# Performance work log

Measured on AMD Instinct MI355X. Metric: run time of the kernel, lower is better.

The kernel has to match this reference:

```python
import jax, jax.numpy as jnp
import numpy as np

D_MODEL = 1024
NHEAD = 16
D_HEAD = D_MODEL // NHEAD


def setup_inputs() -> dict:
    key = jax.random.key(0)
    ks = jax.random.split(key, 9)
    B, S = 2, 2048
    scale = 1.0 / np.sqrt(D_MODEL)
    x = jax.random.normal(ks[0], (B, S, D_MODEL), dtype=jnp.float32)
    Wq = jax.random.normal(ks[1], (D_MODEL, D_MODEL), dtype=jnp.float32) * scale
    Wk = jax.random.normal(ks[2], (D_MODEL, D_MODEL), dtype=jnp.float32) * scale
    Wv = jax.random.normal(ks[3], (D_MODEL, D_MODEL), dtype=jnp.float32) * scale
    Wo = jax.random.normal(ks[4], (D_MODEL, D_MODEL), dtype=jnp.float32) * scale
    bq = jax.random.normal(ks[5], (D_MODEL,), dtype=jnp.float32) * 0.01
    bk = jax.random.normal(ks[6], (D_MODEL,), dtype=jnp.float32) * 0.01
    bv = jax.random.normal(ks[7], (D_MODEL,), dtype=jnp.float32) * 0.01
    bo = jax.random.normal(ks[8], (D_MODEL,), dtype=jnp.float32) * 0.01
    return {"x": x, "Wq": Wq, "bq": bq, "Wk": Wk, "bk": bk,
            "Wv": Wv, "bv": bv, "Wo": Wo, "bo": bo}


def reference(x, Wq, bq, Wk, bk, Wv, bv, Wo, bo):
    B, S, D = x.shape
    H, Dh = NHEAD, D_HEAD
    # projections; weights stored as (in, out) so y = x @ W + b
    def split_heads(t):  # [B,S,D] -> [B,H,S,Dh]
        return t.reshape(B, S, H, Dh).transpose(0, 2, 1, 3)
    q = split_heads(x @ Wq + bq)
    k = split_heads(x @ Wk + bk)
    v = split_heads(x @ Wv + bv)
    scale = 1.0 / jnp.sqrt(jnp.asarray(Dh, dtype=x.dtype))
    attn = jnp.einsum("bhqd,bhkd->bhqk", q, k) * scale  # [B,H,S,S]
    attn = jax.nn.softmax(attn, axis=-1)
    out = jnp.einsum("bhqk,bhkd->bhqd", attn, v)  # [B,H,S,Dh]
    out = out.transpose(0, 2, 1, 3).reshape(B, S, D)
    return out @ Wo + bo
```

## Files before the change

kernel.cpp:

```cpp
#include <hip/hip_runtime.h>
#include <hip/hip_bf16.h>
#include <stdint.h>
#include <stddef.h>

typedef __bf16 b16;
typedef __bf16 b16x4 __attribute__((ext_vector_type(4)));
typedef __bf16 b16x8 __attribute__((ext_vector_type(8)));
typedef float  f32x4 __attribute__((ext_vector_type(4)));

#define LOG2E 1.4426950408889634f
#define QSCALE (0.125f * LOG2E)

#if __has_builtin(__builtin_amdgcn_exp2f)
#define EXP2F(x) __builtin_amdgcn_exp2f(x)
#else
#define EXP2F(x) exp2f(x)
#endif

typedef __attribute__((address_space(1))) void gvoid;
typedef __attribute__((address_space(3))) void svoid;

__device__ __forceinline__ void async_cp16(void* lds, const void* g) {
    __builtin_amdgcn_global_load_lds((gvoid*)(void*)g, (svoid*)lds, 16, 0, 0);
}

__global__ __launch_bounds__(256) void k_cvt_x(const float* __restrict__ x,
                                               b16* __restrict__ xb) {
    int i = (blockIdx.x * 256 + threadIdx.x) * 4;
    float4 v = *(const float4*)(x + i);
    b16x4 o = { (b16)v.x, (b16)v.y, (b16)v.z, (b16)v.w };
    *(b16x4*)(xb + i) = o;
}

__global__ __launch_bounds__(256) void k_transpose(const float* __restrict__ Wq,
                                                   const float* __restrict__ Wk,
                                                   const float* __restrict__ Wv,
                                                   const float* __restrict__ Wo,
                                                   b16* __restrict__ WtQKV,
                                                   b16* __restrict__ Wot) {
    __shared__ float t[32][33];
    const int z = blockIdx.z;
    const float* W = (z == 0) ? Wq : (z == 1) ? Wk : (z == 2) ? Wv : Wo;
    const int k0 = blockIdx.x * 32, n0 = blockIdx.y * 32;
    const int tr = threadIdx.x >> 3, tc4 = (threadIdx.x & 7) * 4;
    float4 v = *(const float4*)(W + (size_t)(k0 + tr) * 1024 + n0 + tc4);
    t[tr][tc4 + 0] = v.x; t[tr][tc4 + 1] = v.y;
    t[tr][tc4 + 2] = v.z; t[tr][tc4 + 3] = v.w;
    __syncthreads();
    b16* dst = (z < 3) ? (WtQKV + ((size_t)z << 20)) : Wot;
    b16x4 o = { (b16)t[tc4 + 0][tr], (b16)t[tc4 + 1][tr],
                (b16)t[tc4 + 2][tr], (b16)t[tc4 + 3][tr] };
    *(b16x4*)(dst + (size_t)(n0 + tr) * 1024 + k0 + tc4) = o;
}

__device__ __forceinline__ void gemm128_core(const b16* __restrict__ Ab,
                                             const b16* __restrict__ Bb,
                                             b16* As, b16* Bs, int tid,
                                             f32x4 acc[4][4]) {
    const int lane = tid & 63, wave = tid >> 6;
    const int wm = wave & 1, wn = wave >> 1;
    const int quad = lane >> 4, lc = lane & 15;
    const int ci0 = tid, ci1 = tid + 256;
    for (int k0 = 0; k0 < 1024; k0 += 32) {
        __syncthreads();
        async_cp16(As + ci0 * 8, Ab + (ci0 >> 2) * 1024 + k0 + (ci0 & 3) * 8);
        async_cp16(As + ci1 * 8, Ab + (ci1 >> 2) * 1024 + k0 + (ci1 & 3) * 8);
        async_cp16(Bs + ci0 * 8, Bb + (ci0 >> 2) * 1024 + k0 + (ci0 & 3) * 8);
        async_cp16(Bs + ci1 * 8, Bb + (ci1 >> 2) * 1024 + k0 + (ci1 & 3) * 8);
        __syncthreads();
        b16x8 af[4], bfr[4];
#pragma unroll
        for (int mt = 0; mt < 4; ++mt)
            af[mt] = *(const b16x8*)(As + (wm * 64 + mt * 16 + lc) * 32 + quad * 8);
#pragma unroll
        for (int nt = 0; nt < 4; ++nt)
            bfr[nt] = *(const b16x8*)(Bs + (wn * 64 + nt * 16 + lc) * 32 + quad * 8);
#pragma unroll
        for (int mt = 0; mt < 4; ++mt)
#pragma unroll
            for (int nt = 0; nt < 4; ++nt)
                acc[mt][nt] = __builtin_amdgcn_mfma_f32_16x16x32_bf16(
                    af[mt], bfr[nt], acc[mt][nt], 0, 0, 0);
    }
}

__global__ __launch_bounds__(256, 2) void k_gemm_qkv(
    const b16* __restrict__ A, const b16* __restrict__ Bt,
    const float* __restrict__ bq, const float* __restrict__ bk,
    const float* __restrict__ bv,
    b16* __restrict__ Qg, b16* __restrict__ Kg, b16* __restrict__ Vtg) {
    __shared__ __align__(16) b16 As[128 * 32];
    __shared__ __align__(16) b16 Bs[128 * 32];
    const int bm = blockIdx.x, bn = blockIdx.y;
    const int tid = threadIdx.x;
    const int lane = tid & 63, wave = tid >> 6;
    const int wm = wave & 1, wn = wave >> 1;
    const int quad = lane >> 4, lc = lane & 15;

    f32x4 acc[4][4] = {};
    gemm128_core(A + (size_t)(bm * 128) * 1024, Bt + (size_t)(bn * 128) * 1024,
                 As, Bs, tid, acc);

    const int mat = bn >> 3;
    const float* bp = (mat == 0) ? bq : (mat == 1) ? bk : bv;
#pragma unroll
    for (int nt = 0; nt < 4; ++nt) {
        const int n = bn * 128 + wn * 64 + nt * 16 + lc;
        const int cm = n & 1023;
        const int h = cm >> 6, dh = cm & 63;
        const float bval = bp[cm];
#pragma unroll
        for (int mt = 0; mt < 4; ++mt) {
            const int m0 = bm * 128 + wm * 64 + mt * 16 + quad * 4;
            const int b = m0 >> 11;
            const int bh = b * 16 + h;
            const int s0 = m0 & 2047;
            if (mat == 2) {
                b16x4 o;
#pragma unroll
                for (int r = 0; r < 4; ++r) o[r] = (b16)(acc[mt][nt][r] + bval);
                *(b16x4*)(Vtg + (size_t)(bh * 64 + dh) * 2048 + s0) = o;
            } else if (mat == 0) {
#pragma unroll
                for (int r = 0; r < 4; ++r)
                    Qg[(size_t)(bh * 2048 + s0 + r) * 64 + dh] =
                        (b16)((acc[mt][nt][r] + bval) * QSCALE);
            } else {
#pragma unroll
                for (int r = 0; r < 4; ++r)
                    Kg[(size_t)(bh * 2048 + s0 + r) * 64 + dh] =
                        (b16)(acc[mt][nt][r] + bval);
            }
        }
    }
}

__global__ __launch_bounds__(256, 2) void k_flash(
    const b16* __restrict__ Qg, const b16* __restrict__ Kg,
    const b16* __restrict__ Vtg,
    float* __restrict__ Opart, float* __restrict__ lpart,
    b16* __restrict__ AO, int ktiles, int direct) {
    __shared__ __align__(16) b16 Ks[64 * 64];
    __shared__ __align__(16) b16 Vs[64 * 64];
    __shared__ __align__(16) b16 Ps[256 * 72];
    const int qb = blockIdx.x;
    const int bh = blockIdx.y;
    const int part = blockIdx.z;
    const int tid = threadIdx.x, lane = tid & 63, wave = tid >> 6;
    const int quad = lane >> 4, lc = lane & 15;

    const b16* Qbase = Qg + ((size_t)bh * 2048 + qb * 256 + wave * 64) * 64;
    b16x8 qf[4][2];
#pragma unroll
    for (int qt = 0; qt < 4; ++qt)
#pragma unroll
        for (int ch = 0; ch < 2; ++ch)
            qf[qt][ch] = *(const b16x8*)(Qbase + (qt * 16 + lc) * 64 + ch * 32 + quad * 8);

    f32x4 oacc[4][4] = {};
    float lsum[4] = {0.f, 0.f, 0.f, 0.f};

    const b16* Kbh = Kg + (size_t)bh * 2048 * 64;
    const b16* Vbh = Vtg + (size_t)bh * 64 * 2048;
    b16* Pw = Ps + wave * (64 * 72);
    const int kt0 = part * ktiles;

    for (int kt = kt0; kt < kt0 + ktiles; ++kt) {
        __syncthreads();
#pragma unroll
        for (int i = 0; i < 2; ++i) {
            const int ci = tid + i * 256;
            const int r = ci >> 3, cs = ci & 7;
            const int gc = cs ^ (r & 7);
            async_cp16(Ks + ci * 8, Kbh + (size_t)(kt * 64 + r) * 64 + gc * 8);
            async_cp16(Vs + ci * 8, Vbh + (size_t)r * 2048 + kt * 64 + gc * 8);
        }
        __syncthreads();

#pragma unroll
        for (int m = 0; m < 4; ++m) {
            b16x8 kf[2];
#pragma unroll
            for (int ch = 0; ch < 2; ++ch) {
                const int row = m * 16 + lc;
                const int chunk = (ch * 4 + quad) ^ (row & 7);
                kf[ch] = *(const b16x8*)(Ks + row * 64 + chunk * 8);
            }
#pragma unroll
            for (int qt = 0; qt < 4; ++qt) {
                f32x4 s = {};
                s = __builtin_amdgcn_mfma_f32_16x16x32_bf16(kf[0], qf[qt][0], s, 0, 0, 0);
                s = __builtin_amdgcn_mfma_f32_16x16x32_bf16(kf[1], qf[qt][1], s, 0, 0, 0);
                float e0 = EXP2F(s[0]), e1 = EXP2F(s[1]);
                float e2 = EXP2F(s[2]), e3 = EXP2F(s[3]);
                lsum[qt] += (e0 + e1) + (e2 + e3);
                b16x4 p = { (b16)e0, (b16)e1, (b16)e2, (b16)e3 };
                *(b16x4*)(Pw + (qt * 16 + lc) * 72 + m * 16 + quad * 4) = p;
            }
        }

#pragma unroll
        for (int ks = 0; ks < 2; ++ks) {
            b16x8 vf[4], pf[4];
#pragma unroll
            for (int dt = 0; dt < 4; ++dt) {
                const int row = dt * 16 + lc;
                const int chunk = (ks * 4 + quad) ^ (row & 7);
                vf[dt] = *(const b16x8*)(Vs + row * 64 + chunk * 8);
            }
#pragma unroll
            for (int mt = 0; mt < 4; ++mt)
                pf[mt] = *(const b16x8*)(Pw + (mt * 16 + lc) * 72 + ks * 32 + quad * 8);
#pragma unroll
            for (int mt = 0; mt < 4; ++mt)
#pragma unroll
                for (int dt = 0; dt < 4; ++dt)
                    oacc[mt][dt] = __builtin_amdgcn_mfma_f32_16x16x32_bf16(
                        pf[mt], vf[dt], oacc[mt][dt], 0, 0, 0);
        }
    }

#pragma unroll
    for (int qt = 0; qt < 4; ++qt) {
        lsum[qt] += __shfl_xor(lsum[qt], 16, 64);
        lsum[qt] += __shfl_xor(lsum[qt], 32, 64);
    }

    if (!direct) {
        float* Op = Opart + ((size_t)(part * 32 + bh) * 2048 + qb * 256 + wave * 64) * 64;
#pragma unroll
        for (int mt = 0; mt < 4; ++mt)
#pragma unroll
            for (int dt = 0; dt < 4; ++dt)
#pragma unroll
                for (int r = 0; r < 4; ++r)
                    Op[(mt * 16 + quad * 4 + r) * 64 + dt * 16 + lc] = oacc[mt][dt][r];
        if (quad == 0) {
            float* lp = lpart + (size_t)(part * 32 + bh) * 2048 + qb * 256 + wave * 64;
#pragma unroll
            for (int qt = 0; qt < 4; ++qt) lp[qt * 16 + lc] = lsum[qt];
        }
    } else {
        float* Ls = (float*)(void*)Pw;
        if (quad == 0) {
#pragma unroll
            for (int qt = 0; qt < 4; ++qt) Ls[qt * 16 + lc] = lsum[qt];
        }
        const int b = bh >> 4, h = bh & 15;
#pragma unroll
        for (int mt = 0; mt < 4; ++mt)
#pragma unroll
            for (int r = 0; r < 4; ++r) {
                const float inv = 1.0f / Ls[mt * 16 + quad * 4 + r];
                const int s = qb * 256 + wave * 64 + mt * 16 + quad * 4 + r;
#pragma unroll
                for (int dt = 0; dt < 4; ++dt)
                    AO[(size_t)(b * 2048 + s) * 1024 + h * 64 + dt * 16 + lc] =
                        (b16)(oacc[mt][dt][r] * inv);
            }
    }
}

__global__ __launch_bounds__(256) void k_merge(const float* __restrict__ Opart,
                                               const float* __restrict__ lpart,
                                               b16* __restrict__ AO, int np) {
    const int bh = blockIdx.y;
    const int q = blockIdx.x * 16 + (threadIdx.x >> 4);
    const int d4 = (threadIdx.x & 15) * 4;
    const size_t qi = (size_t)bh * 2048 + q;
    f32x4 o = *(const f32x4*)(Opart + qi * 64 + d4);
    float l = lpart[qi];
    if (np == 2) {
        o += *(const f32x4*)(Opart + (qi + (size_t)32 * 2048) * 64 + d4);
        l += lpart[qi + (size_t)32 * 2048];
    }
    const float inv = 1.0f / l;
    const int b = bh >> 4, h = bh & 15;
    b16x4 ob = { (b16)(o[0] * inv), (b16)(o[1] * inv),
                 (b16)(o[2] * inv), (b16)(o[3] * inv) };
    *(b16x4*)(AO + (size_t)(b * 2048 + q) * 1024 + h * 64 + d4) = ob;
}

__global__ __launch_bounds__(256, 2) void k_gemm_out(
    const b16* __restrict__ A, const b16* __restrict__ Bt,
    const float* __restrict__ bo, float* __restrict__ out) {
    __shared__ __align__(16) b16 As[128 * 32];
    __shared__ __align__(16) b16 Bs[128 * 32];
    const int bm = blockIdx.x, bn = blockIdx.y;
    const int tid = threadIdx.x;
    const int lane = tid & 63, wave = tid >> 6;
    const int wm = wave & 1, wn = wave >> 1;
    const int quad = lane >> 4, lc = lane & 15;

    f32x4 acc[4][4] = {};
    gemm128_core(A + (size_t)(bm * 128) * 1024, Bt + (size_t)(bn * 128) * 1024,
                 As, Bs, tid, acc);

#pragma unroll
    for (int nt = 0; nt < 4; ++nt) {
        const int n = bn * 128 + wn * 64 + nt * 16 + lc;
        const float bval = bo[n];
#pragma unroll
        for (int mt = 0; mt < 4; ++mt) {
            const int m0 = bm * 128 + wm * 64 + mt * 16 + quad * 4;
#pragma unroll
            for (int r = 0; r < 4; ++r)
                out[(size_t)(m0 + r) * 1024 + n] = acc[mt][nt][r] + bval;
        }
    }
}

extern "C" void kernel_launch(void* const* d_in, const int* in_sizes, int n_in,
                              void* d_out, int out_size, void* d_ws, size_t ws_size,
                              hipStream_t stream) {
    const float* x  = (const float*)d_in[0];
    const float* Wq = (const float*)d_in[1];
    const float* bq = (const float*)d_in[2];
    const float* Wk = (const float*)d_in[3];
    const float* bk = (const float*)d_in[4];
    const float* Wv = (const float*)d_in[5];
    const float* bv = (const float*)d_in[6];
    const float* Wo = (const float*)d_in[7];
    const float* bo = (const float*)d_in[8];
    float* out = (float*)d_out;

    char* ws = (char*)d_ws;
    const size_t MB = 1024 * 1024;
    b16* Xb  = (b16*)(ws);
    b16* AO  = (b16*)(ws);
    b16* WtQ = (b16*)(ws + 8 * MB);
    b16* Wot = (b16*)(ws + 14 * MB);
    b16* Qg  = (b16*)(ws + 16 * MB);
    b16* Kg  = (b16*)(ws + 24 * MB);
    b16* Vtg = (b16*)(ws + 32 * MB);

    const size_t need2 = 40 * MB + 2 * (16 * MB) + 2 * 256 * 1024;
    const int np = (ws_size >= need2) ? 2 : 1;
    float* Opart = (float*)(ws + 40 * MB);
    float* lpart = (float*)(ws + 40 * MB + (size_t)np * 16 * MB);
    const int direct = (np == 1);

    k_cvt_x<<<4096, 256, 0, stream>>>(x, Xb);
    k_transpose<<<dim3(32, 32, 4), 256, 0, stream>>>(Wq, Wk, Wv, Wo, WtQ, Wot);
    k_gemm_qkv<<<dim3(32, 24), 256, 0, stream>>>(Xb, WtQ, bq, bk, bv, Qg, Kg, Vtg);
    k_flash<<<dim3(8, 32, np), 256, 0, stream>>>(Qg, Kg, Vtg, Opart, lpart, AO,
                                                 32 / np, direct);
    if (!direct)
        k_merge<<<dim3(128, 32), 256, 0, stream>>>(Opart, lpart, AO, np);
    k_gemm_out<<<dim3(32, 8), 256, 0, stream>>>(AO, Wot, bo, out);
}
```

Before: 200.0 us.

## Double-buffer K/V tiles in flash kernel with async prefetch and swizzled P

The flash attention kernel now double-buffers K and V tiles in LDS. It issues the async global-to-LDS copy for the next tile before computing on the current one and waits with explicit vmcnt counters instead of two __syncthreads per tile. The P scratch buffer moves from padded rows to an XOR-swizzled layout, which saves LDS while avoiding bank conflicts. MFMA sections get raised wave priority, and the grid is flattened to 1D so that blocks sharing the same q-block and different heads or parts are scheduled adjacently. The extra K/V buffers raise LDS use, and the hand-coded waitcnt depends on the exact count of outstanding loads.

```diff
diff --git a/kernel.cpp b/kernel.cpp
--- a/kernel.cpp
+++ b/kernel.cpp
@@ -135,20 +135,45 @@
     }
 }
 
+__device__ __forceinline__ void flash_stage(b16* Kd, b16* Vd,
+                                            const b16* __restrict__ Kbh,
+                                            const b16* __restrict__ Vbh,
+                                            int kt, int tid) {
+#pragma unroll
+    for (int i = 0; i < 2; ++i) {
+        const int ci = tid + i * 256;
+        const int r = ci >> 3, cs = ci & 7;
+        const int gc = cs ^ (r & 7);
+        async_cp16(Kd + ci * 8, Kbh + (size_t)(kt * 64 + r) * 64 + gc * 8);
+        async_cp16(Vd + ci * 8, Vbh + (size_t)r * 2048 + kt * 64 + gc * 8);
+    }
+}
+
 __global__ __launch_bounds__(256, 2) void k_flash(
     const b16* __restrict__ Qg, const b16* __restrict__ Kg,
     const b16* __restrict__ Vtg,
     float* __restrict__ Opart, float* __restrict__ lpart,
-    b16* __restrict__ AO, int ktiles, int direct) {
-    __shared__ __align__(16) b16 Ks[64 * 64];
-    __shared__ __align__(16) b16 Vs[64 * 64];
-    __shared__ __align__(16) b16 Ps[256 * 72];
-    const int qb = blockIdx.x;
-    const int bh = blockIdx.y;
-    const int part = blockIdx.z;
+    b16* __restrict__ AO, int ktiles, int direct, int np) {
+    __shared__ __align__(16) b16 Ks[2 * 64 * 64];
+    __shared__ __align__(16) b16 Vs[2 * 64 * 64];
+    __shared__ __align__(16) b16 Ps[256 * 64];
+
+    const int bid = blockIdx.x;
+    const int gstride = np << 5;
+    const int qb = bid / gstride;
+    const int rem = bid - qb * gstride;
+    const int bh = rem / np;
+    const int part = rem - bh * np;
+
     const int tid = threadIdx.x, lane = tid & 63, wave = tid >> 6;
     const int quad = lane >> 4, lc = lane & 15;
 
+    const b16* Kbh = Kg + (size_t)bh * 2048 * 64;
+    const b16* Vbh = Vtg + (size_t)bh * 64 * 2048;
+    const int kt0 = part * ktiles, ktE = kt0 + ktiles;
+
+    flash_stage(Ks, Vs, Kbh, Vbh, kt0, tid);
+
     const b16* Qbase = Qg + ((size_t)bh * 2048 + qb * 256 + wave * 64) * 64;
     b16x8 qf[4][2];
 #pragma unroll
@@ -159,23 +184,22 @@
 
     f32x4 oacc[4][4] = {};
     float lsum[4] = {0.f, 0.f, 0.f, 0.f};
-
-    const b16* Kbh = Kg + (size_t)bh * 2048 * 64;
-    const b16* Vbh = Vtg + (size_t)bh * 64 * 2048;
-    b16* Pw = Ps + wave * (64 * 72);
-    const int kt0 = part * ktiles;
-
-    for (int kt = kt0; kt < kt0 + ktiles; ++kt) {
-        __syncthreads();
-#pragma unroll
-        for (int i = 0; i < 2; ++i) {
-            const int ci = tid + i * 256;
-            const int r = ci >> 3, cs = ci & 7;
-            const int gc = cs ^ (r & 7);
-            async_cp16(Ks + ci * 8, Kbh + (size_t)(kt * 64 + r) * 64 + gc * 8);
-            async_cp16(Vs + ci * 8, Vbh + (size_t)r * 2048 + kt * 64 + gc * 8);
-        }
-        __syncthreads();
+    b16* Pw = Ps + wave * 4096;
+
+    for (int kt = kt0; kt < ktE; ++kt) {
+        const int cur = (kt - kt0) & 1;
+        const b16* Kc = Ks + cur * 4096;
+        const b16* Vc = Vs + cur * 4096;
+
+        if (kt + 1 < ktE) {
+            flash_stage(Ks + (cur ^ 1) * 4096, Vs + (cur ^ 1) * 4096,
+                        Kbh, Vbh, kt + 1, tid);
+            asm volatile("s_waitcnt vmcnt(4)" ::: "memory");
+        } else {
+            asm volatile("s_waitcnt vmcnt(0)" ::: "memory");
+        }
+        __builtin_amdgcn_s_barrier();
+        __builtin_amdgcn_sched_barrier(0);
 
 #pragma unroll
         for (int m = 0; m < 4; ++m) {
@@ -184,18 +208,22 @@
             for (int ch = 0; ch < 2; ++ch) {
                 const int row = m * 16 + lc;
                 const int chunk = (ch * 4 + quad) ^ (row & 7);
-                kf[ch] = *(const b16x8*)(Ks + row * 64 + chunk * 8);
+                kf[ch] = *(const b16x8*)(Kc + row * 64 + chunk * 8);
             }
 #pragma unroll
             for (int qt = 0; qt < 4; ++qt) {
                 f32x4 s = {};
+                __builtin_amdgcn_s_setprio(1);
                 s = __builtin_amdgcn_mfma_f32_16x16x32_bf16(kf[0], qf[qt][0], s, 0, 0, 0);
                 s = __builtin_amdgcn_mfma_f32_16x16x32_bf16(kf[1], qf[qt][1], s, 0, 0, 0);
+                __builtin_amdgcn_s_setprio(0);
                 float e0 = EXP2F(s[0]), e1 = EXP2F(s[1]);
                 float e2 = EXP2F(s[2]), e3 = EXP2F(s[3]);
                 lsum[qt] += (e0 + e1) + (e2 + e3);
                 b16x4 p = { (b16)e0, (b16)e1, (b16)e2, (b16)e3 };
-                *(b16x4*)(Pw + (qt * 16 + lc) * 72 + m * 16 + quad * 4) = p;
+                const int prow = qt * 16 + lc;
+                const int pbyte = (prow * 128 + m * 32 + quad * 8) ^ ((prow & 7) << 4);
+                *(b16x4*)((char*)Pw + pbyte) = p;
             }
         }
 
@@ -206,18 +234,26 @@
             for (int dt = 0; dt < 4; ++dt) {
                 const int row = dt * 16 + lc;
                 const int chunk = (ks * 4 + quad) ^ (row & 7);
-                vf[dt] = *(const b16x8*)(Vs + row * 64 + chunk * 8);
-            }
-#pragma unroll
-            for (int mt = 0; mt < 4; ++mt)
-                pf[mt] = *(const b16x8*)(Pw + (mt * 16 + lc) * 72 + ks * 32 + quad * 8);
+                vf[dt] = *(const b16x8*)(Vc + row * 64 + chunk * 8);
+            }
+#pragma unroll
+            for (int mt = 0; mt < 4; ++mt) {
+                const int prow = mt * 16 + lc;
+                const int pbyte = (prow * 128 + ks * 64 + quad * 16) ^ ((prow & 7) << 4);
+                pf[mt] = *(const b16x8*)((const char*)Pw + pbyte);
+            }
+            __builtin_amdgcn_s_setprio(1);
 #pragma unroll
             for (int mt = 0; mt < 4; ++mt)
 #pragma unroll
                 for (int dt = 0; dt < 4; ++dt)
                     oacc[mt][dt] = __builtin_amdgcn_mfma_f32_16x16x32_bf16(
                         pf[mt], vf[dt], oacc[mt][dt], 0, 0, 0);
-        }
+            __builtin_amdgcn_s_setprio(0);
+        }
+
+        __builtin_amdgcn_sched_barrier(0);
+        __builtin_amdgcn_s_barrier();
     }
 
 #pragma unroll
@@ -343,8 +379,8 @@
     k_cvt_x<<<4096, 256, 0, stream>>>(x, Xb);
     k_transpose<<<dim3(32, 32, 4), 256, 0, stream>>>(Wq, Wk, Wv, Wo, WtQ, Wot);
     k_gemm_qkv<<<dim3(32, 24), 256, 0, stream>>>(Xb, WtQ, bq, bk, bv, Qg, Kg, Vtg);
-    k_flash<<<dim3(8, 32, np), 256, 0, stream>>>(Qg, Kg, Vtg, Opart, lpart, AO,
-                                                 32 / np, direct);
+    k_flash<<<dim3(8 * 32 * np), 256, 0, stream>>>(Qg, Kg, Vtg, Opart, lpart, AO,
+                                                   32 / np, direct, np);
     if (!direct)
         k_merge<<<dim3(128, 32), 256, 0, stream>>>(Opart, lpart, AO, np);
     k_gemm_out<<<dim3(32, 8), 256, 0, stream>>>(AO, Wot, bo, out);
```

Result: faster. 196.0 us (-2.0%).
